# Optimization experiments

Hardware: AMD Instinct MI355X
Metric: run time of the kernel (lower is better)

The kernel has to match this reference:

```python
import jax, jax.numpy as jnp
import numpy as np

VOCAB = 256
EMBED = 128
HIDDEN = 512
BATCH = 64
SEQ = 1024


def setup_inputs() -> dict:
    key = jax.random.key(0)
    ks = jax.random.split(key, 6)
    x = jax.random.randint(ks[0], (BATCH, SEQ), 0, VOCAB)
    hidden = jnp.zeros((BATCH, HIDDEN), dtype=jnp.float32)
    embedding = jax.random.normal(ks[1], (VOCAB, EMBED), dtype=jnp.float32)
    W_xh = jax.random.normal(ks[2], (EMBED, HIDDEN), dtype=jnp.float32) * 0.01
    W_hh = jax.random.normal(ks[3], (HIDDEN, HIDDEN), dtype=jnp.float32) * 0.01
    b_h = jnp.zeros((HIDDEN,), dtype=jnp.float32)
    # nn.Linear(hidden, vocab): weight [vocab, hidden], bias [vocab]
    W_hy_w = jax.random.normal(ks[4], (VOCAB, HIDDEN), dtype=jnp.float32) * (1.0 / np.sqrt(HIDDEN))
    W_hy_b = jax.random.normal(ks[5], (VOCAB,), dtype=jnp.float32) * 0.01
    return {"x": x, "hidden": hidden, "embedding": embedding, "W_xh": W_xh,
            "W_hh": W_hh, "b_h": b_h, "W_hy_w": W_hy_w, "W_hy_b": W_hy_b}


def reference(x, hidden, embedding, W_xh, W_hh, b_h, W_hy_w, W_hy_b):
    # x: [b, l] int tokens -> embed: [b, l, e]
    x_embed = embedding[x]
    # Precompute input projections in one batched GEMM: [l, b, h]
    xw = jnp.einsum('ble,eh->lbh', x_embed, W_xh) + b_h

    def step(h, xw_t):
        h_new = jnp.tanh(xw_t + h @ W_hh)
        return h_new, h_new

    final_hidden, outs = jax.lax.scan(step, hidden, xw)  # outs: [l, b, h]
    outs = jnp.transpose(outs, (1, 0, 2))  # [b, l, h]
    logits = outs @ W_hy_w.T + W_hy_b  # [b, l, vocab]
    return logits, final_hidden
```

## Files before the change

kernel.cpp:

```cpp
#include <hip/hip_runtime.h>
#include <hip/hip_bf16.h>
#include <stdint.h>

#define BATCH  64
#define SEQ    1024
#define EMBED  128
#define HIDDEN 512
#define VOCAB  256

using bf16 = __hip_bfloat16;
typedef __attribute__((ext_vector_type(8))) short bf16x8;
typedef __attribute__((ext_vector_type(4))) float f32x4;

__device__ __forceinline__ float bfu(unsigned short u) {
    return __uint_as_float(((unsigned)u) << 16);
}

__global__ void k_cvt(const float* __restrict__ in, bf16* __restrict__ out, int n) {
    int i = blockIdx.x * 256 + threadIdx.x;
    if (i < n) out[i] = __float2bfloat16(in[i]);
}

__global__ void k_txp_wxh(const float* __restrict__ in, bf16* __restrict__ out) {
    int idx = blockIdx.x * 256 + threadIdx.x;
    int e = idx >> 9, j = idx & 511;
    out[j * EMBED + e] = __float2bfloat16(in[idx]);
}

__global__ void k_txp_whh(const float* __restrict__ in, bf16* __restrict__ out) {
    int idx = blockIdx.x * 256 + threadIdx.x;
    int k = idx >> 9, n = idx & 511;
    out[n * HIDDEN + k] = __float2bfloat16(in[idx]);
}

template<bool GATHER, bool OUT_BF16, bool PERMUTE>
__global__ __launch_bounds__(256) void k_gemm(
    const bf16* __restrict__ A,
    const int*  __restrict__ xtok,
    const bf16* __restrict__ B,
    const float* __restrict__ bias,
    float* __restrict__ Cf,
    bf16*  __restrict__ Cb,
    int M, int N, int K)
{
    __shared__ bf16 As[64][72];
    __shared__ bf16 Bs[64][72];
    const int m0 = blockIdx.x * 64, n0 = blockIdx.y * 64;
    const int tid  = threadIdx.x;
    const int lane = tid & 63, wid = tid >> 6;
    const int wm = wid >> 1, wn = wid & 1;
    const int lrow = tid >> 3, lc8 = tid & 7;

    f32x4 acc[2][2] = {};

    for (int k0 = 0; k0 < K; k0 += 64) {
#pragma unroll
        for (int pass = 0; pass < 2; ++pass) {
            int row = pass * 32 + lrow;
            const bf16* asrc;
            if (GATHER) {
                int m = m0 + row;
                int t = m >> 6, bb = m & 63;
                int tok = xtok[bb * SEQ + t];
                asrc = A + (size_t)tok * K + k0 + lc8 * 8;
            } else {
                asrc = A + (size_t)(m0 + row) * K + k0 + lc8 * 8;
            }
            *reinterpret_cast<uint4*>(&As[row][lc8 * 8]) = *reinterpret_cast<const uint4*>(asrc);
            *reinterpret_cast<uint4*>(&Bs[row][lc8 * 8]) =
                *reinterpret_cast<const uint4*>(B + (size_t)(n0 + row) * K + k0 + lc8 * 8);
        }
        __syncthreads();
#pragma unroll
        for (int kk = 0; kk < 2; ++kk) {
            bf16x8 af[2], bg[2];
#pragma unroll
            for (int mt = 0; mt < 2; ++mt)
                af[mt] = *reinterpret_cast<const bf16x8*>(
                    &As[wm * 32 + mt * 16 + (lane & 15)][kk * 32 + (lane >> 4) * 8]);
#pragma unroll
            for (int nt = 0; nt < 2; ++nt)
                bg[nt] = *reinterpret_cast<const bf16x8*>(
                    &Bs[wn * 32 + nt * 16 + (lane & 15)][kk * 32 + (lane >> 4) * 8]);
#pragma unroll
            for (int mt = 0; mt < 2; ++mt)
#pragma unroll
                for (int nt = 0; nt < 2; ++nt)
                    acc[mt][nt] = __builtin_amdgcn_mfma_f32_16x16x32_bf16(
                        af[mt], bg[nt], acc[mt][nt], 0, 0, 0);
        }
        __syncthreads();
    }
    if (PERMUTE) {
        const int t = m0 >> 6;
        const int wid_s = (n0 >> 5) + wn;
#pragma unroll
        for (int mt = 0; mt < 2; ++mt) {
            int blk = wm * 2 + mt;
            bf16 tmp[8];
#pragma unroll
            for (int nt = 0; nt < 2; ++nt) {
                int col = n0 + wn * 32 + nt * 16 + (lane & 15);
                float bv = bias[col];
#pragma unroll
                for (int r = 0; r < 4; ++r)
                    tmp[nt * 4 + r] = __float2bfloat16(acc[mt][nt][r] + bv);
            }
            size_t off = ((size_t)(t * 4 + blk) * 1024 +
                          wid_s * 64 + (lane >> 4) * 16 + (lane & 15)) * 8;
            *reinterpret_cast<uint4*>(Cb + off) = *reinterpret_cast<uint4*>(tmp);
        }
    } else {
#pragma unroll
        for (int mt = 0; mt < 2; ++mt) {
            int rbase = m0 + wm * 32 + mt * 16 + (lane >> 4) * 4;
#pragma unroll
            for (int nt = 0; nt < 2; ++nt) {
                int col = n0 + wn * 32 + nt * 16 + (lane & 15);
                float bv = bias[col];
#pragma unroll
                for (int r = 0; r < 4; ++r) {
                    float v = acc[mt][nt][r] + bv;
                    size_t off = (size_t)(rbase + r) * N + col;
                    if (OUT_BF16) Cb[off] = __float2bfloat16(v);
                    else          Cf[off] = v;
                }
            }
        }
    }
}

#define ROWS 16
#define CHK_LDS 3
#define CHK_REG 8
#define WRES_STRIDE (CHK_LDS * 32 + 8)
#define H_STRIDE (HIDDEN + 8)

__global__ __launch_bounds__(1024, 4) void k_scan_mfma(
    const bf16* __restrict__ xwp,
    const bf16* __restrict__ wt,
    const float* __restrict__ h0,
    bf16* __restrict__ hh,
    float* __restrict__ hfin)
{
    __shared__ bf16 wres[HIDDEN * WRES_STRIDE];
    __shared__ bf16 h_lds[2][ROWS * H_STRIDE];

    const int tid  = threadIdx.x;
    const int lane = tid & 63, wid = tid >> 6;
    const int b0   = blockIdx.x * ROWS;
    const int scol = wid * 32;
    const int lm   = lane & 15, lk = lane >> 4;

    {
        int row = tid >> 1, half = tid & 1;
        const bf16* src = wt + (size_t)row * HIDDEN + half * 48;
        bf16* dst = &wres[row * WRES_STRIDE + half * 48];
#pragma unroll
        for (int j = 0; j < 6; ++j)
            *reinterpret_cast<uint4*>(dst + j * 8) =
                *reinterpret_cast<const uint4*>(src + j * 8);
    }
    {
        int row = tid >> 6, c = (tid & 63) * 8;
        const float* src = h0 + (size_t)(b0 + row) * HIDDEN + c;
        bf16 tmp[8];
#pragma unroll
        for (int j = 0; j < 8; ++j) tmp[j] = __float2bfloat16(src[j]);
        *reinterpret_cast<uint4*>(&h_lds[0][row * H_STRIDE + c]) =
            *reinterpret_cast<uint4*>(&tmp[0]);
    }

    bf16x8 breg[CHK_REG][2];
#pragma unroll
    for (int c = 0; c < CHK_REG; ++c)
#pragma unroll
        for (int nt = 0; nt < 2; ++nt) {
            breg[c][nt] = *reinterpret_cast<const bf16x8*>(
                wt + (size_t)(scol + nt * 16 + lm) * HIDDEN + (CHK_LDS + c) * 32 + lk * 8);
            asm volatile("" : "+v"(breg[c][nt]));
        }

    const bf16* grow[2];
    const bf16* lrowp[2];
#pragma unroll
    for (int nt = 0; nt < 2; ++nt) {
        int row = scol + nt * 16 + lm;
        grow[nt]  = wt + (size_t)row * HIDDEN + lk * 8;
        lrowp[nt] = &wres[row * WRES_STRIDE + lk * 8];
    }

    const int srow = tid >> 6, sc = (tid & 63) * 8;

    __syncthreads();

    int p = 0;
    for (int t = 0; t < SEQ; ++t) {
        if (t > 0) {
            uint4 v0 = *reinterpret_cast<const uint4*>(&h_lds[p][srow * H_STRIDE + sc]);
            bf16* dst = hh + ((size_t)(b0 + srow) * SEQ + (t - 1)) * HIDDEN + sc;
            *reinterpret_cast<uint4*>(dst) = v0;
        }

        ushort xe[8];
        *reinterpret_cast<uint4*>(&xe[0]) =
            *(reinterpret_cast<const uint4*>(xwp) +
              (size_t)(t * 4 + blockIdx.x) * 1024 + tid);

        f32x4 acc[2] = {};
#pragma unroll
        for (int kc = 0; kc < 16; ++kc) {
            bf16x8 af = *reinterpret_cast<const bf16x8*>(
                &h_lds[p][lm * H_STRIDE + kc * 32 + lk * 8]);
#pragma unroll
            for (int nt = 0; nt < 2; ++nt) {
                bf16x8 bg;
                if (kc < CHK_LDS)
                    bg = *reinterpret_cast<const bf16x8*>(lrowp[nt] + kc * 32);
                else if (kc < CHK_LDS + CHK_REG)
                    bg = breg[kc - CHK_LDS][nt];
                else
                    bg = *reinterpret_cast<const bf16x8*>(grow[nt] + kc * 32);
                acc[nt] = __builtin_amdgcn_mfma_f32_16x16x32_bf16(af, bg, acc[nt], 0, 0, 0);
            }
        }

#pragma unroll
        for (int nt = 0; nt < 2; ++nt) {
            int col = scol + nt * 16 + lm;
#pragma unroll
            for (int r = 0; r < 4; ++r) {
                int m = lk * 4 + r;
                float pre = acc[nt][r] + bfu(xe[nt * 4 + r]);
                float e2  = __expf(2.f * pre);
                float hn  = 1.f - 2.f / (e2 + 1.f);
                h_lds[p ^ 1][m * H_STRIDE + col] = __float2bfloat16(hn);
                if (t == SEQ - 1) hfin[(size_t)(b0 + m) * HIDDEN + col] = hn;
            }
        }
        p ^= 1;
        __syncthreads();
    }

    {
        uint4 v0 = *reinterpret_cast<const uint4*>(&h_lds[p][srow * H_STRIDE + sc]);
        bf16* dst = hh + ((size_t)(b0 + srow) * SEQ + (SEQ - 1)) * HIDDEN + sc;
        *reinterpret_cast<uint4*>(dst) = v0;
    }
}

extern "C" void kernel_launch(void* const* d_in, const int* in_sizes, int n_in,
                              void* d_out, int out_size, void* d_ws, size_t ws_size,
                              hipStream_t stream) {
    const int*   x    = (const int*)  d_in[0];
    const float* h0   = (const float*)d_in[1];
    const float* emb  = (const float*)d_in[2];
    const float* wxh  = (const float*)d_in[3];
    const float* whh  = (const float*)d_in[4];
    const float* bh   = (const float*)d_in[5];
    const float* whyw = (const float*)d_in[6];
    const float* whyb = (const float*)d_in[7];

    float* logits = (float*)d_out;
    float* hfin   = logits + (size_t)BATCH * SEQ * VOCAB;

    char* p = (char*)d_ws;
    bf16* xwp    = (bf16*)p; p += (size_t)SEQ * BATCH * HIDDEN * 2;
    bf16* hh     = (bf16*)p; p += (size_t)BATCH * SEQ * HIDDEN * 2;
    bf16* wt     = (bf16*)p; p += (size_t)HIDDEN * HIDDEN * 2;
    bf16* wxh_t  = (bf16*)p; p += (size_t)HIDDEN * EMBED * 2;
    bf16* emb_bf = (bf16*)p; p += (size_t)VOCAB * EMBED * 2;
    bf16* why_bf = (bf16*)p; p += (size_t)VOCAB * HIDDEN * 2;

    k_txp_whh<<<(HIDDEN * HIDDEN + 255) / 256, 256, 0, stream>>>(whh, wt);
    k_cvt<<<(VOCAB * EMBED + 255) / 256, 256, 0, stream>>>(emb, emb_bf, VOCAB * EMBED);
    k_cvt<<<(VOCAB * HIDDEN + 255) / 256, 256, 0, stream>>>(whyw, why_bf, VOCAB * HIDDEN);
    k_txp_wxh<<<(EMBED * HIDDEN + 255) / 256, 256, 0, stream>>>(wxh, wxh_t);

    k_gemm<true, true, true><<<dim3((SEQ * BATCH) / 64, HIDDEN / 64), 256, 0, stream>>>(
        emb_bf, x, wxh_t, bh, nullptr, xwp, SEQ * BATCH, HIDDEN, EMBED);

    k_scan_mfma<<<BATCH / ROWS, 1024, 0, stream>>>(xwp, wt, h0, hh, hfin);

    k_gemm<false, false, false><<<dim3((BATCH * SEQ) / 64, VOCAB / 64), 256, 0, stream>>>(
        hh, nullptr, why_bf, whyb, logits, nullptr, BATCH * SEQ, VOCAB, HIDDEN);
}
```

Measured before the change: 2.939 ms.

## Swizzle hidden-state LDS layout and drop LDS-resident weight chunks

Replaces the padded row-major hidden-state LDS buffer with a chunk-major layout that uses an XOR-like permutation. MFMA A-fragment loads and the tanh write-back then map to contiguous, conflict-reduced addresses. The three weight chunks previously staged in LDS are removed. Register-resident chunks now cover k-chunks 0-7 and the remaining 8 are read from global/cache each step. The final hidden-state fp32 write moves out of the time loop and is rebuilt from the bf16 state, which adds rounding error to hfin. The aim is cheaper LDS traffic on the serial critical path, at the cost of more global weight loads per step.

```diff
diff --git a/kernel.cpp b/kernel.cpp
--- a/kernel.cpp
+++ b/kernel.cpp
@@ -14,6 +14,9 @@
 
 __device__ __forceinline__ float bfu(unsigned short u) {
     return __uint_as_float(((unsigned)u) << 16);
+}
+__device__ __forceinline__ int pib(int b) {
+    return (b & 32) | ((b & 3) << 3) | ((b >> 2) & 7);
 }
 
 __global__ void k_cvt(const float* __restrict__ in, bf16* __restrict__ out, int n) {
@@ -131,10 +134,7 @@
 }
 
 #define ROWS 16
-#define CHK_LDS 3
 #define CHK_REG 8
-#define WRES_STRIDE (CHK_LDS * 32 + 8)
-#define H_STRIDE (HIDDEN + 8)
 
 __global__ __launch_bounds__(1024, 4) void k_scan_mfma(
     const bf16* __restrict__ xwp,
@@ -143,8 +143,7 @@
     bf16* __restrict__ hh,
     float* __restrict__ hfin)
 {
-    __shared__ bf16 wres[HIDDEN * WRES_STRIDE];
-    __shared__ bf16 h_lds[2][ROWS * H_STRIDE];
+    __shared__ bf16 hp[2][16 * 512];
 
     const int tid  = threadIdx.x;
     const int lane = tid & 63, wid = tid >> 6;
@@ -152,23 +151,15 @@
     const int scol = wid * 32;
     const int lm   = lane & 15, lk = lane >> 4;
 
+    const int srow = tid >> 6, sc = (tid & 63) * 8;
+    const int raddr = (sc >> 5) * 512 + pib(((sc & 31) >> 3) * 16 + srow) * 8;
+
     {
-        int row = tid >> 1, half = tid & 1;
-        const bf16* src = wt + (size_t)row * HIDDEN + half * 48;
-        bf16* dst = &wres[row * WRES_STRIDE + half * 48];
-#pragma unroll
-        for (int j = 0; j < 6; ++j)
-            *reinterpret_cast<uint4*>(dst + j * 8) =
-                *reinterpret_cast<const uint4*>(src + j * 8);
-    }
-    {
-        int row = tid >> 6, c = (tid & 63) * 8;
-        const float* src = h0 + (size_t)(b0 + row) * HIDDEN + c;
+        const float* src = h0 + (size_t)(b0 + srow) * HIDDEN + sc;
         bf16 tmp[8];
 #pragma unroll
         for (int j = 0; j < 8; ++j) tmp[j] = __float2bfloat16(src[j]);
-        *reinterpret_cast<uint4*>(&h_lds[0][row * H_STRIDE + c]) =
-            *reinterpret_cast<uint4*>(&tmp[0]);
+        *reinterpret_cast<uint4*>(&hp[0][raddr]) = *reinterpret_cast<uint4*>(&tmp[0]);
     }
 
     bf16x8 breg[CHK_REG][2];
@@ -177,29 +168,25 @@
 #pragma unroll
         for (int nt = 0; nt < 2; ++nt) {
             breg[c][nt] = *reinterpret_cast<const bf16x8*>(
-                wt + (size_t)(scol + nt * 16 + lm) * HIDDEN + (CHK_LDS + c) * 32 + lk * 8);
+                wt + (size_t)(scol + nt * 16 + lm) * HIDDEN + c * 32 + lk * 8);
             asm volatile("" : "+v"(breg[c][nt]));
         }
 
     const bf16* grow[2];
-    const bf16* lrowp[2];
-#pragma unroll
-    for (int nt = 0; nt < 2; ++nt) {
-        int row = scol + nt * 16 + lm;
-        grow[nt]  = wt + (size_t)row * HIDDEN + lk * 8;
-        lrowp[nt] = &wres[row * WRES_STRIDE + lk * 8];
-    }
-
-    const int srow = tid >> 6, sc = (tid & 63) * 8;
+#pragma unroll
+    for (int nt = 0; nt < 2; ++nt)
+        grow[nt] = wt + (size_t)(scol + nt * 16 + lm) * HIDDEN + lk * 8;
+
+    const int abase = pib(lane) * 8;
 
     __syncthreads();
 
     int p = 0;
     for (int t = 0; t < SEQ; ++t) {
         if (t > 0) {
-            uint4 v0 = *reinterpret_cast<const uint4*>(&h_lds[p][srow * H_STRIDE + sc]);
-            bf16* dst = hh + ((size_t)(b0 + srow) * SEQ + (t - 1)) * HIDDEN + sc;
-            *reinterpret_cast<uint4*>(dst) = v0;
+            uint4 v = *reinterpret_cast<const uint4*>(&hp[p][raddr]);
+            *reinterpret_cast<uint4*>(
+                hh + ((size_t)(b0 + srow) * SEQ + (t - 1)) * HIDDEN + sc) = v;
         }
 
         ushort xe[8];
@@ -209,43 +196,45 @@
 
         f32x4 acc[2] = {};
 #pragma unroll
-        for (int kc = 0; kc < 16; ++kc) {
-            bf16x8 af = *reinterpret_cast<const bf16x8*>(
-                &h_lds[p][lm * H_STRIDE + kc * 32 + lk * 8]);
-#pragma unroll
-            for (int nt = 0; nt < 2; ++nt) {
-                bf16x8 bg;
-                if (kc < CHK_LDS)
-                    bg = *reinterpret_cast<const bf16x8*>(lrowp[nt] + kc * 32);
-                else if (kc < CHK_LDS + CHK_REG)
-                    bg = breg[kc - CHK_LDS][nt];
-                else
-                    bg = *reinterpret_cast<const bf16x8*>(grow[nt] + kc * 32);
-                acc[nt] = __builtin_amdgcn_mfma_f32_16x16x32_bf16(af, bg, acc[nt], 0, 0, 0);
-            }
-        }
-
-#pragma unroll
-        for (int nt = 0; nt < 2; ++nt) {
-            int col = scol + nt * 16 + lm;
-#pragma unroll
-            for (int r = 0; r < 4; ++r) {
-                int m = lk * 4 + r;
-                float pre = acc[nt][r] + bfu(xe[nt * 4 + r]);
-                float e2  = __expf(2.f * pre);
-                float hn  = 1.f - 2.f / (e2 + 1.f);
-                h_lds[p ^ 1][m * H_STRIDE + col] = __float2bfloat16(hn);
-                if (t == SEQ - 1) hfin[(size_t)(b0 + m) * HIDDEN + col] = hn;
-            }
+        for (int kc = 0; kc < CHK_REG; ++kc) {
+            bf16x8 af = *reinterpret_cast<const bf16x8*>(&hp[p][kc * 512 + abase]);
+            acc[0] = __builtin_amdgcn_mfma_f32_16x16x32_bf16(af, breg[kc][0], acc[0], 0, 0, 0);
+            acc[1] = __builtin_amdgcn_mfma_f32_16x16x32_bf16(af, breg[kc][1], acc[1], 0, 0, 0);
+        }
+#pragma unroll
+        for (int kc = CHK_REG; kc < 16; ++kc) {
+            bf16x8 af  = *reinterpret_cast<const bf16x8*>(&hp[p][kc * 512 + abase]);
+            bf16x8 bg0 = *reinterpret_cast<const bf16x8*>(grow[0] + kc * 32);
+            bf16x8 bg1 = *reinterpret_cast<const bf16x8*>(grow[1] + kc * 32);
+            acc[0] = __builtin_amdgcn_mfma_f32_16x16x32_bf16(af, bg0, acc[0], 0, 0, 0);
+            acc[1] = __builtin_amdgcn_mfma_f32_16x16x32_bf16(af, bg1, acc[1], 0, 0, 0);
+        }
+
+        {
+            bf16* hw = &hp[p ^ 1][wid * 512];
+#pragma unroll
+            for (int nt = 0; nt < 2; ++nt)
+#pragma unroll
+                for (int r = 0; r < 4; ++r) {
+                    float pre = acc[nt][r] + bfu(xe[nt * 4 + r]);
+                    float e2  = __expf(2.f * pre);
+                    float hn  = 1.f - 2.f / (e2 + 1.f);
+                    int blk = (nt * 2 + (lm >> 3)) * 16 + lk * 4 + r;
+                    hw[pib(blk) * 8 + (lm & 7)] = __float2bfloat16(hn);
+                }
         }
         p ^= 1;
         __syncthreads();
     }
 
     {
-        uint4 v0 = *reinterpret_cast<const uint4*>(&h_lds[p][srow * H_STRIDE + sc]);
-        bf16* dst = hh + ((size_t)(b0 + srow) * SEQ + (SEQ - 1)) * HIDDEN + sc;
-        *reinterpret_cast<uint4*>(dst) = v0;
+        uint4 v = *reinterpret_cast<const uint4*>(&hp[p][raddr]);
+        *reinterpret_cast<uint4*>(
+            hh + ((size_t)(b0 + srow) * SEQ + (SEQ - 1)) * HIDDEN + sc) = v;
+        const ushort* u = reinterpret_cast<const ushort*>(&v);
+        float* dst = hfin + (size_t)(b0 + srow) * HIDDEN + sc;
+#pragma unroll
+        for (int j = 0; j < 8; ++j) dst[j] = bfu(u[j]);
     }
 }
 
```

After: 4.606 ms. 56.7% more time.
